# Kernel tuning notes

Hardware: AMD Instinct MI355X
Metric: run time of the kernel (lower is better)

The kernel has to match this reference:

```python
import jax, jax.numpy as jnp
import numpy as np

LEAKY_SLOPE = 0.2   # LeakyReLU alpha from __init__
MASK_VAL = -9e15    # matches torch -9000000000000000.0


def setup_inputs() -> dict:
    key = jax.random.key(0)
    ks = jax.random.split(key, 11)
    B, N, L, D = 64, 512, 50, 128
    return {
        "h_locs_l": jax.random.normal(ks[0], (B, L, D), jnp.float32),
        "h_times_l": jax.random.normal(ks[1], (B, L, D), jnp.float32),
        "int_emb": jax.random.normal(ks[2], (B, L, D), jnp.float32),
        "h": jax.random.normal(ks[3], (B, N, D), jnp.float32),
        "adj": jax.random.randint(ks[4], (B, N, N), 0, 5, jnp.int32),
        "wd": jax.random.normal(ks[5], (D, D), jnp.float32),
        "a_0": jax.random.normal(ks[6], (D, 1), jnp.float32),
        "a_1": jax.random.normal(ks[7], (D, 1), jnp.float32),
        "a_2": jax.random.normal(ks[8], (D, 1), jnp.float32),
        "a_3": jax.random.normal(ks[9], (D, 1), jnp.float32),
        "bias": jax.random.normal(ks[10], (D,), jnp.float32),  # declared but unused in forward
    }


def reference(h_locs_l, h_times_l, int_emb, h, adj, wd, a_0, a_1, a_2, a_3, bias):
    # h: [B,N,D]; adj: [B,N,N] int relation types
    # h_ds = mean over concatenated aux sequences, projected by wd -> [B,D]
    h_ds = jnp.mean(jnp.concatenate([h_locs_l, h_times_l, int_emb], axis=1), axis=1) @ wd

    hd = h * h_ds[:, None, :]  # [B,N,D] = h_i * h_ds

    def scores(a):
        # a_input[b,i,j] = h_i*h_ds + h_j*h_ds + h_i*h_j ; e = leakyrelu(a_input @ a)
        # Decompose: rank-1 row/col terms + generalized gram term (never build [B,N,N,D]).
        a = a[:, 0]                                  # [D]
        s = hd @ a                                   # [B,N]
        cross = jnp.einsum('bid,bjd,d->bij', h, h, a)  # [B,N,N]
        e = s[:, :, None] + s[:, None, :] + cross
        return jax.nn.leaky_relu(e, LEAKY_SLOPE)

    e_0, e_1, e_2, e_3 = scores(a_0), scores(a_1), scores(a_2), scores(a_3)

    alpha = jnp.full_like(e_0, MASK_VAL)
    alpha = jnp.where(adj == 1, e_0, alpha)
    alpha = jnp.where(adj == 2, e_1, alpha)
    alpha = jnp.where(adj == 3, e_2, alpha)
    alpha = jnp.where(adj == 4, e_3, alpha)
    alpha = jax.nn.softmax(alpha, axis=-1)
    return jnp.matmul(alpha, h)  # [B,N,D]
```

## Files before the change

### kernel.cpp

```cpp
#include <hip/hip_runtime.h>
#include <hip/hip_bf16.h>
#include <hip/hip_fp16.h>

typedef _Float16 half8 __attribute__((ext_vector_type(8)));
typedef float floatx4 __attribute__((ext_vector_type(4)));
typedef unsigned short u16;
typedef unsigned int u32;
typedef unsigned long long u64;

#define LEAKY 0.2f
#define MASKV -9.0e15f

__global__ __launch_bounds__(256) void k_hds(const float* __restrict__ hl,
                                             const float* __restrict__ ht,
                                             const float* __restrict__ ie,
                                             const float* __restrict__ wd,
                                             float* __restrict__ hds) {
  int b = blockIdx.x, tid = threadIdx.x;
  int d = tid & 127, hh = tid >> 7;
  __shared__ float pa_[2][128];
  __shared__ float ml[128];
  __shared__ float pb_[2][128];
  const size_t base = (size_t)b * 50 * 128 + d;
  float acc = 0.f;
  for (int r = hh * 25; r < hh * 25 + 25; ++r) {
    size_t o = base + (size_t)r * 128;
    acc += hl[o] + ht[o] + ie[o];
  }
  pa_[hh][d] = acc;
  __syncthreads();
  if (hh == 0) ml[d] = (pa_[0][d] + pa_[1][d]) * (1.0f / 150.0f);
  __syncthreads();
  float o = 0.f;
  for (int k = hh * 64; k < hh * 64 + 64; ++k) o = fmaf(ml[k], wd[k * 128 + d], o);
  pb_[hh][d] = o;
  __syncthreads();
  if (hh == 0) hds[b * 128 + d] = pb_[0][d] + pb_[1][d];
}

__global__ __launch_bounds__(256) void k_prep(const float* __restrict__ h,
                                              const float* __restrict__ hds,
                                              const float* __restrict__ a0,
                                              const float* __restrict__ a1,
                                              const float* __restrict__ a2,
                                              const float* __restrict__ a3,
                                              float* __restrict__ s,
                                              u16* __restrict__ h16,
                                              u16* __restrict__ h16T) {
  int b = blockIdx.x >> 3, i0 = (blockIdx.x & 7) * 64;
  int tid = threadIdx.x, w = tid >> 6, l = tid & 63;
  __shared__ u16 tile[64][130];
  int d0 = 2 * l;
  float2 hd2 = *(const float2*)(hds + b * 128 + d0);
  float2 av0 = *(const float2*)(a0 + d0);
  float2 av1 = *(const float2*)(a1 + d0);
  float2 av2 = *(const float2*)(a2 + d0);
  float2 av3 = *(const float2*)(a3 + d0);
  for (int rr = 0; rr < 16; ++rr) {
    int il = rr * 4 + w;
    size_t row = (size_t)b * 512 + i0 + il;
    float2 hv = *(const float2*)(h + row * 128 + d0);
    _Float16 f0 = (_Float16)hv.x, f1 = (_Float16)hv.y;
    u16 u0 = __builtin_bit_cast(u16, f0), u1 = __builtin_bit_cast(u16, f1);
    tile[il][d0] = u0;
    tile[il][d0 + 1] = u1;
    *(u32*)(h16 + row * 128 + d0) = (u32)u0 | ((u32)u1 << 16);
    float t0 = hv.x * hd2.x, t1 = hv.y * hd2.y;
    float p0 = t0 * av0.x + t1 * av0.y;
    float p1 = t0 * av1.x + t1 * av1.y;
    float p2 = t0 * av2.x + t1 * av2.y;
    float p3 = t0 * av3.x + t1 * av3.y;
    for (int off = 32; off >= 1; off >>= 1) {
      p0 += __shfl_xor(p0, off);
      p1 += __shfl_xor(p1, off);
      p2 += __shfl_xor(p2, off);
      p3 += __shfl_xor(p3, off);
    }
    if (l < 4) {
      float pw = (l == 0) ? p0 : (l == 1) ? p1 : (l == 2) ? p2 : p3;
      s[((size_t)l * 64 + b) * 512 + i0 + il] = pw;
    }
  }
  __syncthreads();
  int d = tid >> 1, hf = tid & 1;
  u32 wds[16];
#pragma unroll
  for (int k = 0; k < 16; ++k) {
    u32 lo = tile[32 * hf + 2 * k][d];
    u32 hi = tile[32 * hf + 2 * k + 1][d];
    wds[k] = lo | (hi << 16);
  }
  uint4* dst = (uint4*)(h16T + ((size_t)b * 128 + d) * 512 + i0 + 32 * hf);
  dst[0] = make_uint4(wds[0], wds[1], wds[2], wds[3]);
  dst[1] = make_uint4(wds[4], wds[5], wds[6], wds[7]);
  dst[2] = make_uint4(wds[8], wds[9], wds[10], wds[11]);
  dst[3] = make_uint4(wds[12], wds[13], wds[14], wds[15]);
}

__global__ __launch_bounds__(256, 3) void k_attn(const u16* __restrict__ h16,
                                                 const u16* __restrict__ h16T,
                                                 const float* __restrict__ s,
                                                 const int* __restrict__ adj,
                                                 const float* __restrict__ a0,
                                                 const float* __restrict__ a1,
                                                 const float* __restrict__ a2,
                                                 const float* __restrict__ a3,
                                                 float* __restrict__ out) {
  int bid = blockIdx.x;
  int wg = (bid & 7) * 256 + (bid >> 3);
  int b = wg >> 5, i0r = (wg & 31) * 16;
  int tid = threadIdx.x, jq = tid >> 6, l = tid & 63;
  int l15 = l & 15, l4 = l >> 4;

  __shared__ u16 a16[4][128];
  __shared__ float s_lds[4][512];
  __shared__ u16 pbuf[4][16][40];
  __shared__ float mrg[4][16][132];
  __shared__ float mml[4][16][2];

  const size_t hb16 = (size_t)b * 512 * 128;
  const size_t hTb = (size_t)b * 128 * 512;

  half8 hf[4];
#pragma unroll
  for (int ks = 0; ks < 4; ++ks)
    hf[ks] = *(const half8*)(h16 + hb16 + (size_t)(i0r + l15) * 128 + ks * 32 + 8 * l4);

  if (tid < 128) {
    a16[0][tid] = __builtin_bit_cast(u16, (_Float16)a0[tid]);
    a16[1][tid] = __builtin_bit_cast(u16, (_Float16)a1[tid]);
    a16[2][tid] = __builtin_bit_cast(u16, (_Float16)a2[tid]);
    a16[3][tid] = __builtin_bit_cast(u16, (_Float16)a3[tid]);
  }
#pragma unroll
  for (int p = 0; p < 2; ++p) {
    int cid = p * 256 + tid;
    int hd = cid >> 7, i4 = (cid & 127) * 4;
    *(float4*)&s_lds[hd][i4] = *(const float4*)(s + ((size_t)hd * 64 + b) * 512 + i4);
  }
  __syncthreads();

  float m[4], lsum[4];
#pragma unroll
  for (int e = 0; e < 4; ++e) { m[e] = MASKV; lsum[e] = 0.f; }
  floatx4 pv[8];
#pragma unroll
  for (int dt = 0; dt < 8; ++dt) pv[dt] = (floatx4){0.f, 0.f, 0.f, 0.f};

  for (int t = 0; t < 4; ++t) {
    const int j0 = jq * 128 + 32 * t;

    int av[2][4];
#pragma unroll
    for (int e = 0; e < 4; ++e) {
      const int* ar = adj + ((size_t)(b * 512 + i0r + 4 * l4 + e)) * 512 + j0 + l15;
      av[0][e] = ar[0];
      av[1][e] = ar[16];
    }

    half8 kfa[8];
#pragma unroll
    for (int ks = 0; ks < 4; ++ks)
#pragma unroll
      for (int C = 0; C < 2; ++C)
        kfa[ks * 2 + C] = *(const half8*)(h16 + hb16 + (size_t)(j0 + 16 * C + l15) * 128 + ks * 32 + 8 * l4);

    float x[2][4];
#pragma unroll
    for (int C = 0; C < 2; ++C)
#pragma unroll
      for (int e = 0; e < 4; ++e) x[C][e] = MASKV;

    for (int hd = 0; hd < 4; ++hd) {
      floatx4 qk[2];
      qk[0] = (floatx4){0.f, 0.f, 0.f, 0.f};
      qk[1] = (floatx4){0.f, 0.f, 0.f, 0.f};
      __builtin_amdgcn_s_setprio(1);
#pragma unroll
      for (int ks = 0; ks < 4; ++ks) {
        half8 af = *(const half8*)&a16[hd][ks * 32 + 8 * l4];
        half8 q = hf[ks] * af;
        qk[0] = __builtin_amdgcn_mfma_f32_16x16x32_f16(q, kfa[ks * 2 + 0], qk[0], 0, 0, 0);
        qk[1] = __builtin_amdgcn_mfma_f32_16x16x32_f16(q, kfa[ks * 2 + 1], qk[1], 0, 0, 0);
      }
      __builtin_amdgcn_s_setprio(0);
#pragma unroll
      for (int C = 0; C < 2; ++C) {
        float sjh = s_lds[hd][j0 + 16 * C + l15];
#pragma unroll
        for (int e = 0; e < 4; ++e) {
          if (av[C][e] == hd + 1) {
            float v = qk[C][e] + s_lds[hd][i0r + 4 * l4 + e] + sjh;
            x[C][e] = (v > 0.f) ? v : LEAKY * v;
          }
        }
      }
    }

    half8 vba[8];
#pragma unroll
    for (int dt = 0; dt < 8; ++dt)
      vba[dt] = *(const half8*)(h16T + hTb + (size_t)(16 * dt + l15) * 512 + j0 + 8 * l4);

#pragma unroll
    for (int e = 0; e < 4; ++e) {
      float tmax = fmaxf(x[0][e], x[1][e]);
      tmax = fmaxf(tmax, __shfl_xor(tmax, 1));
      tmax = fmaxf(tmax, __shfl_xor(tmax, 2));
      tmax = fmaxf(tmax, __shfl_xor(tmax, 4));
      tmax = fmaxf(tmax, __shfl_xor(tmax, 8));
      float mn = fmaxf(m[e], tmax);
      float sc = __expf(m[e] - mn);
      float p0 = __expf(x[0][e] - mn);
      float p1 = __expf(x[1][e] - mn);
      float ls = p0 + p1;
      ls += __shfl_xor(ls, 1);
      ls += __shfl_xor(ls, 2);
      ls += __shfl_xor(ls, 4);
      ls += __shfl_xor(ls, 8);
      lsum[e] = lsum[e] * sc + ls;
      m[e] = mn;
#pragma unroll
      for (int dt = 0; dt < 8; ++dt) pv[dt][e] *= sc;
      int r = 4 * l4 + e;
      pbuf[jq][r][0 + l15] = __builtin_bit_cast(u16, (_Float16)p0);
      pbuf[jq][r][16 + l15] = __builtin_bit_cast(u16, (_Float16)p1);
    }

    asm volatile("s_waitcnt lgkmcnt(0)" ::: "memory");
    __builtin_amdgcn_sched_barrier(0);

    half8 pa = *(const half8*)((const char*)&pbuf[jq][0][0] + l15 * 80 + l4 * 16);
    __builtin_amdgcn_s_setprio(1);
#pragma unroll
    for (int dt = 0; dt < 8; ++dt)
      pv[dt] = __builtin_amdgcn_mfma_f32_16x16x32_f16(pa, vba[dt], pv[dt], 0, 0, 0);
    __builtin_amdgcn_s_setprio(0);
  }

#pragma unroll
  for (int dt = 0; dt < 8; ++dt)
#pragma unroll
    for (int e = 0; e < 4; ++e)
      mrg[jq][4 * l4 + e][16 * dt + l15] = pv[dt][e];
  if (l15 == 0) {
#pragma unroll
    for (int e = 0; e < 4; ++e) {
      mml[jq][4 * l4 + e][0] = m[e];
      mml[jq][4 * l4 + e][1] = lsum[e];
    }
  }
  __syncthreads();

  for (int p2 = 0; p2 < 2; ++p2) {
    int i = (tid >> 5) + 8 * p2;
    int dc = (tid & 31) * 4;
    float m0 = mml[0][i][0], m1 = mml[1][i][0], m2 = mml[2][i][0], m3 = mml[3][i][0];
    float M = fmaxf(fmaxf(m0, m1), fmaxf(m2, m3));
    float w0 = __expf(m0 - M), w1 = __expf(m1 - M), w2 = __expf(m2 - M), w3 = __expf(m3 - M);
    float L = mml[0][i][1] * w0 + mml[1][i][1] * w1 + mml[2][i][1] * w2 + mml[3][i][1] * w3;
    float inv = 1.0f / L;
    w0 *= inv; w1 *= inv; w2 *= inv; w3 *= inv;
    float4 v0 = *(float4*)&mrg[0][i][dc];
    float4 v1 = *(float4*)&mrg[1][i][dc];
    float4 v2 = *(float4*)&mrg[2][i][dc];
    float4 v3 = *(float4*)&mrg[3][i][dc];
    float4 o;
    o.x = v0.x * w0 + v1.x * w1 + v2.x * w2 + v3.x * w3;
    o.y = v0.y * w0 + v1.y * w1 + v2.y * w2 + v3.y * w3;
    o.z = v0.z * w0 + v1.z * w1 + v2.z * w2 + v3.z * w3;
    o.w = v0.w * w0 + v1.w * w1 + v2.w * w2 + v3.w * w3;
    *(float4*)(out + ((size_t)b * 512 + i0r + i) * 128 + dc) = o;
  }
}

extern "C" void kernel_launch(void* const* d_in, const int* in_sizes, int n_in,
                              void* d_out, int out_size, void* d_ws, size_t ws_size,
                              hipStream_t stream) {
  const float* hl = (const float*)d_in[0];
  const float* ht = (const float*)d_in[1];
  const float* ie = (const float*)d_in[2];
  const float* h  = (const float*)d_in[3];
  const int* adj  = (const int*)d_in[4];
  const float* wd = (const float*)d_in[5];
  const float* a0 = (const float*)d_in[6];
  const float* a1 = (const float*)d_in[7];
  const float* a2 = (const float*)d_in[8];
  const float* a3 = (const float*)d_in[9];

  float* hds  = (float*)d_ws;
  float* s    = (float*)((char*)d_ws + 32768);
  u16* h16    = (u16*)((char*)d_ws + 557056);
  u16* h16T   = (u16*)((char*)d_ws + 8945664);
  float* o    = (float*)d_out;

  k_hds<<<64, 256, 0, stream>>>(hl, ht, ie, wd, hds);
  k_prep<<<512, 256, 0, stream>>>(h, hds, a0, a1, a2, a3, s, h16, h16T);
  k_attn<<<2048, 256, 0, stream>>>(h16, h16T, s, adj, a0, a1, a2, a3, o);
}
```

Baseline: 100.6 us.

## Raise attention occupancy by staging query rows in LDS and halving merge buffer

```diff
diff --git a/kernel.cpp b/kernel.cpp
--- a/kernel.cpp
+++ b/kernel.cpp
@@ -97,7 +97,7 @@
   dst[3] = make_uint4(wds[12], wds[13], wds[14], wds[15]);
 }
 
-__global__ __launch_bounds__(256, 3) void k_attn(const u16* __restrict__ h16,
+__global__ __launch_bounds__(256, 4) void k_attn(const u16* __restrict__ h16,
                                                  const u16* __restrict__ h16T,
                                                  const float* __restrict__ s,
                                                  const int* __restrict__ adj,
@@ -114,17 +114,13 @@
 
   __shared__ u16 a16[4][128];
   __shared__ float s_lds[4][512];
+  __shared__ u16 hrow[16][136];
   __shared__ u16 pbuf[4][16][40];
-  __shared__ float mrg[4][16][132];
+  __shared__ u16 mrg_h[4][16][136];
   __shared__ float mml[4][16][2];
 
   const size_t hb16 = (size_t)b * 512 * 128;
   const size_t hTb = (size_t)b * 128 * 512;
-
-  half8 hf[4];
-#pragma unroll
-  for (int ks = 0; ks < 4; ++ks)
-    hf[ks] = *(const half8*)(h16 + hb16 + (size_t)(i0r + l15) * 128 + ks * 32 + 8 * l4);
 
   if (tid < 128) {
     a16[0][tid] = __builtin_bit_cast(u16, (_Float16)a0[tid]);
@@ -138,6 +134,10 @@
     int hd = cid >> 7, i4 = (cid & 127) * 4;
     *(float4*)&s_lds[hd][i4] = *(const float4*)(s + ((size_t)hd * 64 + b) * 512 + i4);
   }
+  {
+    int row = tid >> 4, ch = tid & 15;
+    *(uint4*)&hrow[row][ch * 8] = *(const uint4*)(h16 + hb16 + (size_t)(i0r + row) * 128 + ch * 8);
+  }
   __syncthreads();
 
   float m[4], lsum[4];
@@ -158,39 +158,42 @@
       av[1][e] = ar[16];
     }
 
-    half8 kfa[8];
-#pragma unroll
-    for (int ks = 0; ks < 4; ++ks)
-#pragma unroll
-      for (int C = 0; C < 2; ++C)
-        kfa[ks * 2 + C] = *(const half8*)(h16 + hb16 + (size_t)(j0 + 16 * C + l15) * 128 + ks * 32 + 8 * l4);
-
-    float x[2][4];
-#pragma unroll
-    for (int C = 0; C < 2; ++C)
-#pragma unroll
-      for (int e = 0; e < 4; ++e) x[C][e] = MASKV;
-
+    floatx4 qk[4][2];
+#pragma unroll
     for (int hd = 0; hd < 4; ++hd) {
-      floatx4 qk[2];
-      qk[0] = (floatx4){0.f, 0.f, 0.f, 0.f};
-      qk[1] = (floatx4){0.f, 0.f, 0.f, 0.f};
+      qk[hd][0] = (floatx4){0.f, 0.f, 0.f, 0.f};
+      qk[hd][1] = (floatx4){0.f, 0.f, 0.f, 0.f};
+    }
+#pragma unroll
+    for (int ks = 0; ks < 4; ++ks) {
+      half8 kf0 = *(const half8*)(h16 + hb16 + (size_t)(j0 + l15) * 128 + ks * 32 + 8 * l4);
+      half8 kf1 = *(const half8*)(h16 + hb16 + (size_t)(j0 + 16 + l15) * 128 + ks * 32 + 8 * l4);
+      half8 hfr = *(const half8*)((const char*)&hrow[0][0] + l15 * 272 + ks * 64 + l4 * 16);
       __builtin_amdgcn_s_setprio(1);
 #pragma unroll
-      for (int ks = 0; ks < 4; ++ks) {
+      for (int hd = 0; hd < 4; ++hd) {
         half8 af = *(const half8*)&a16[hd][ks * 32 + 8 * l4];
-        half8 q = hf[ks] * af;
-        qk[0] = __builtin_amdgcn_mfma_f32_16x16x32_f16(q, kfa[ks * 2 + 0], qk[0], 0, 0, 0);
-        qk[1] = __builtin_amdgcn_mfma_f32_16x16x32_f16(q, kfa[ks * 2 + 1], qk[1], 0, 0, 0);
+        half8 q = hfr * af;
+        qk[hd][0] = __builtin_amdgcn_mfma_f32_16x16x32_f16(q, kf0, qk[hd][0], 0, 0, 0);
+        qk[hd][1] = __builtin_amdgcn_mfma_f32_16x16x32_f16(q, kf1, qk[hd][1], 0, 0, 0);
       }
       __builtin_amdgcn_s_setprio(0);
+    }
+
+    float x[2][4];
+#pragma unroll
+    for (int C = 0; C < 2; ++C)
+#pragma unroll
+      for (int e = 0; e < 4; ++e) x[C][e] = MASKV;
+#pragma unroll
+    for (int hd = 0; hd < 4; ++hd) {
 #pragma unroll
       for (int C = 0; C < 2; ++C) {
         float sjh = s_lds[hd][j0 + 16 * C + l15];
 #pragma unroll
         for (int e = 0; e < 4; ++e) {
           if (av[C][e] == hd + 1) {
-            float v = qk[C][e] + s_lds[hd][i0r + 4 * l4 + e] + sjh;
+            float v = qk[hd][C][e] + s_lds[hd][i0r + 4 * l4 + e] + sjh;
             x[C][e] = (v > 0.f) ? v : LEAKY * v;
           }
         }
@@ -242,7 +245,7 @@
   for (int dt = 0; dt < 8; ++dt)
 #pragma unroll
     for (int e = 0; e < 4; ++e)
-      mrg[jq][4 * l4 + e][16 * dt + l15] = pv[dt][e];
+      mrg_h[jq][4 * l4 + e][16 * dt + l15] = __builtin_bit_cast(u16, (_Float16)pv[dt][e]);
   if (l15 == 0) {
 #pragma unroll
     for (int e = 0; e < 4; ++e) {
@@ -261,15 +264,16 @@
     float L = mml[0][i][1] * w0 + mml[1][i][1] * w1 + mml[2][i][1] * w2 + mml[3][i][1] * w3;
     float inv = 1.0f / L;
     w0 *= inv; w1 *= inv; w2 *= inv; w3 *= inv;
-    float4 v0 = *(float4*)&mrg[0][i][dc];
-    float4 v1 = *(float4*)&mrg[1][i][dc];
-    float4 v2 = *(float4*)&mrg[2][i][dc];
-    float4 v3 = *(float4*)&mrg[3][i][dc];
-    float4 o;
-    o.x = v0.x * w0 + v1.x * w1 + v2.x * w2 + v3.x * w3;
-    o.y = v0.y * w0 + v1.y * w1 + v2.y * w2 + v3.y * w3;
-    o.z = v0.z * w0 + v1.z * w1 + v2.z * w2 + v3.z * w3;
-    o.w = v0.w * w0 + v1.w * w1 + v2.w * w2 + v3.w * w3;
+    float4 o = make_float4(0.f, 0.f, 0.f, 0.f);
+    const float wq[4] = {w0, w1, w2, w3};
+#pragma unroll
+    for (int q = 0; q < 4; ++q) {
+      ushort4 hv = *(const ushort4*)&mrg_h[q][i][dc];
+      o.x += wq[q] * (float)__builtin_bit_cast(_Float16, hv.x);
+      o.y += wq[q] * (float)__builtin_bit_cast(_Float16, hv.y);
+      o.z += wq[q] * (float)__builtin_bit_cast(_Float16, hv.z);
+      o.w += wq[q] * (float)__builtin_bit_cast(_Float16, hv.w);
+    }
     *(float4*)(out + ((size_t)b * 512 + i0r + i) * 128 + dc) = o;
   }
 }
```

Result: faster. 98.28 us, median of 2 (-2.3%).
